# Optimization experiments

Measured on AMD Instinct MI355X. Metric: run time of the kernel, lower is better.

Reference implementation:

```python
import jax, jax.numpy as jnp
import numpy as np

B, S, D, H = 2, 2048, 1024, 16
HD = D // H


def setup_inputs() -> dict:
    key = jax.random.key(0)
    ks = jax.random.split(key, 9)
    s = 1.0 / np.sqrt(D)
    return {
        "qx": jax.random.normal(ks[0], (B, S, D), jnp.float32),
        "kx": jax.random.normal(ks[1], (B, S, D), jnp.float32),
        "vx": jax.random.normal(ks[2], (B, S, D), jnp.float32),
        "mask": jnp.tril(jnp.ones((S, S), jnp.int32))[None, None],  # [1,1,S,S] causal
        "Wq": jax.random.uniform(ks[3], (D, D), jnp.float32, -s, s),
        "bq": jax.random.uniform(ks[4], (D,), jnp.float32, -s, s),
        "Wk": jax.random.uniform(ks[5], (D, D), jnp.float32, -s, s),
        "bk": jax.random.uniform(ks[6], (D,), jnp.float32, -s, s),
        "Wv": jax.random.uniform(ks[7], (D, D), jnp.float32, -s, s),
        "bv": jax.random.uniform(ks[8], (D,), jnp.float32, -s, s),
    }


def reference(qx, kx, vx, mask, Wq, bq, Wk, bk, Wv, bv):
    bat, seq_len, d_model = qx.shape
    # torch Linear: y = x @ W.T + b
    q = qx @ Wq.T + bq
    k = kx @ Wk.T + bk
    v = vx @ Wv.T + bv
    # [b, h, s, hd]
    q = q.reshape(bat, seq_len, H, HD).transpose(0, 2, 1, 3)
    k = k.reshape(bat, seq_len, H, HD).transpose(0, 2, 1, 3)
    v = v.reshape(bat, seq_len, H, HD).transpose(0, 2, 1, 3)
    # NOTE: original scales by sqrt(d_model), not sqrt(head_dim)
    attn_weight = jnp.einsum('bhqd,bhkd->bhqk', q, k) / jnp.sqrt(
        jnp.asarray(d_model, q.dtype))
    attn_weight = jnp.where(mask == 0, -jnp.inf, attn_weight)
    attn_score = jax.nn.softmax(attn_weight, axis=-1)
    attn_output = jnp.einsum('bhqk,bhkd->bhqd', attn_score, v)
    return attn_output.transpose(0, 2, 1, 3).reshape(bat, seq_len, d_model)
```

## Files before the change

kernel.cpp:

```cpp
#include <hip/hip_runtime.h>


typedef __attribute__((ext_vector_type(8))) short short8;
typedef __attribute__((ext_vector_type(4))) short shortx4;
typedef __attribute__((ext_vector_type(4))) float floatx4;

#define NEGBIG (-1.0e30f)
#define QSCALE 0.04508422002778011f

__device__ __forceinline__ float bf2f(ushort u) {
    union { unsigned int i; float f; } x; x.i = ((unsigned int)u) << 16; return x.f;
}
__device__ __forceinline__ ushort f2bf(float f) {
    union { unsigned int i; float f; } x; x.f = f;
    return (ushort)((x.i + 0x7FFFu + ((x.i >> 16) & 1u)) >> 16);
}
__device__ __forceinline__ ushort f2bf_trunc(float f) {
    union { unsigned int i; float f; } x; x.f = f;
    return (ushort)(x.i >> 16);
}
__device__ __forceinline__ void gl_lds16(const void* g, void* l) {
    __builtin_amdgcn_global_load_lds(
        (const __attribute__((address_space(1))) unsigned int*)g,
        (__attribute__((address_space(3))) unsigned int*)l, 16, 0, 0);
}

__global__ void convert_fp32(
    const float* __restrict__ qx, const float* __restrict__ kx, const float* __restrict__ vx,
    const float* __restrict__ wq, const float* __restrict__ wk, const float* __restrict__ wv,
    const float* __restrict__ bq, const float* __restrict__ bk, const float* __restrict__ bv,
    ushort* __restrict__ dst, int* __restrict__ flag)
{
    const unsigned int* w = (const unsigned int*)qx;
    int hits = 0;
#pragma unroll
    for (int i = 0; i < 4; ++i) {
        unsigned int v = w[threadIdx.x * 4 + i];
        int e = (int)((v >> 7) & 0xFF);
        hits += (e >= 100 && e <= 135) ? 1 : 0;
    }
    __shared__ int red[4];
    for (int off = 32; off; off >>= 1) hits += __shfl_down(hits, off);
    if ((threadIdx.x & 63) == 0) red[threadIdx.x >> 6] = hits;
    __syncthreads();
    const int dt = (red[0] + red[1] + red[2] + red[3] > 512) ? 1 : 0;
    if (blockIdx.x == 0 && threadIdx.x == 0) *flag = dt;
    if (dt) return;

    const int v = blockIdx.x * 256 + threadIdx.x;
    const float* src; int off = v;
    if      (v < 1048576) { src = qx; }
    else if (v < 2097152) { src = kx; off = v - 1048576; }
    else if (v < 3145728) { src = vx; off = v - 2097152; }
    else if (v < 3407872) { src = wq; off = v - 3145728; }
    else if (v < 3670016) { src = wk; off = v - 3407872; }
    else if (v < 3932160) { src = wv; off = v - 3670016; }
    else if (v < 3932416) { src = bq; off = v - 3932160; }
    else if (v < 3932672) { src = bk; off = v - 3932416; }
    else                  { src = bv; off = v - 3932672; }
    float4 f = ((const float4*)src)[off];
    shortx4 o;
    o[0] = (short)f2bf(f.x); o[1] = (short)f2bf(f.y);
    o[2] = (short)f2bf(f.z); o[3] = (short)f2bf(f.w);
    *(shortx4*)&dst[(size_t)v * 4] = o;
}

__global__ __launch_bounds__(256, 4) void qkv_gemm(
    const void* __restrict__ Xq_, const void* __restrict__ Wq_, const void* __restrict__ bq_,
    const void* __restrict__ Xk_, const void* __restrict__ Wk_, const void* __restrict__ bk_,
    const void* __restrict__ Xv_, const void* __restrict__ Wv_, const void* __restrict__ bv_,
    const ushort* __restrict__ conv,
    ushort* __restrict__ Yq, ushort* __restrict__ Yk, ushort* __restrict__ Yv,
    const int* __restrict__ flag)
{
    const int idx = blockIdx.x;
    const int xcd = idx & 7;
    const int j   = (idx >> 3) & 7;
    const int pg  = idx >> 6;
    const int p   = pg * 8 + xcd;
    const int z   = p >> 5;
    const int m0  = (p & 31) * 128;
    const int n0  = j * 128;

    const int dt = *flag;
    const ushort* X = dt ? (const ushort*)(z == 0 ? Xq_ : z == 1 ? Xk_ : Xv_)
                         : conv + (size_t)z * 4194304;
    const ushort* W = dt ? (const ushort*)(z == 0 ? Wq_ : z == 1 ? Wk_ : Wv_)
                         : conv + 12582912 + (size_t)z * 1048576;
    const ushort* bias = dt ? (const ushort*)(z == 0 ? bq_ : z == 1 ? bk_ : bv_)
                            : conv + 15728640 + z * 1024;
    ushort* Y = (z == 0) ? Yq : (z == 1) ? Yk : Yv;
    const float oscale = (z == 0) ? QSCALE : 1.0f;

    __shared__ __align__(16) ushort As[128 * 64];
    __shared__ __align__(16) ushort Bs[128 * 64];

    const int tid  = threadIdx.x;
    const int wave = tid >> 6;
    const int lane = tid & 63;
    const int col  = lane & 15;
    const int quad = lane >> 4;
    const int wm   = (wave >> 1) * 64;
    const int wn   = (wave & 1) * 64;

    floatx4 acc[4][4] = {};

    for (int k0 = 0; k0 < 1024; k0 += 64) {
        __syncthreads();
#pragma unroll
        for (int c = 0; c < 4; ++c) {
            const int o   = c * 4096 + tid * 16;
            const int row = o >> 7;
            const int bg  = ((o >> 4) & 7) ^ (row & 7);
            gl_lds16(X + (size_t)(m0 + row) * 1024 + k0 + bg * 8, &As[o >> 1]);
            gl_lds16(W + (size_t)(n0 + row) * 1024 + k0 + bg * 8, &Bs[o >> 1]);
        }
        __syncthreads();

#pragma unroll
        for (int h = 0; h < 2; ++h) {
            short8 af[4], bf_[4];
#pragma unroll
            for (int i = 0; i < 4; ++i) {
                const int ra = wm + i * 16 + col;
                const int rb = wn + i * 16 + col;
                af[i]  = *(const short8*)&As[ra * 64 + (((h * 4 + quad) ^ (ra & 7)) * 8)];
                bf_[i] = *(const short8*)&Bs[rb * 64 + (((h * 4 + quad) ^ (rb & 7)) * 8)];
            }
#pragma unroll
            for (int i = 0; i < 4; ++i)
#pragma unroll
                for (int jj = 0; jj < 4; ++jj)
                    acc[i][jj] = __builtin_amdgcn_mfma_f32_16x16x32_bf16(af[i], bf_[jj], acc[i][jj], 0, 0, 0);
        }
    }

    if (z == 2) {
#pragma unroll
        for (int jj = 0; jj < 4; ++jj) {
            const int n = n0 + wn + jj * 16 + col;
            const float bb = bf2f(bias[n]);
#pragma unroll
            for (int i = 0; i < 4; ++i) {
                const int m = m0 + wm + i * 16 + quad * 4;
                shortx4 pk;
#pragma unroll
                for (int r = 0; r < 4; ++r) pk[r] = (short)f2bf(acc[i][jj][r] + bb);
                *(shortx4*)&Y[((size_t)(m >> 11) * 1024 + n) * 2048 + (m & 2047)] = pk;
            }
        }
    } else {
#pragma unroll
        for (int jj = 0; jj < 4; ++jj) {
            const int n = n0 + wn + jj * 16 + col;
            const float bb = bf2f(bias[n]);
#pragma unroll
            for (int i = 0; i < 4; ++i)
#pragma unroll
                for (int r = 0; r < 4; ++r) {
                    const int m = m0 + wm + i * 16 + quad * 4 + r;
                    Y[(size_t)m * 1024 + n] = f2bf((acc[i][jj][r] + bb) * oscale);
                }
        }
    }
}

#define LDP 72

__global__ __launch_bounds__(256, 4) void attn(
    const ushort* __restrict__ Q, const ushort* __restrict__ K,
    const ushort* __restrict__ Vt, void* __restrict__ O,
    const int* __restrict__ flag)
{
    const int i   = blockIdx.x;
    const int xcd = i & 7;
    const int i3  = i >> 3;
    const int run = i3 >> 5;
    const int p   = i3 & 31;
    const int qt0 = (p & 1) ? (p >> 1) : (31 - (p >> 1));
    const int qt  = (run & 1) ? (31 - qt0) : qt0;
    const int g   = xcd + 8 * run;
    const int b   = g >> 4;
    const int h   = g & 15;
    const int q0  = qt * 64;
    const int dt  = *flag;

    __shared__ __align__(16) ushort Qs[64 * 64];
    __shared__ __align__(16) ushort Ks[64 * 64];
    __shared__ __align__(16) ushort Vs[64 * 64];
    __shared__ __align__(16) ushort Ps[4][16 * LDP];

    const int tid  = threadIdx.x;
    const int wave = tid >> 6;
    const int lane = tid & 63;
    const int col  = lane & 15;
    const int quad = lane >> 4;

    const size_t qkbase = ((size_t)b * 2048) * 1024 + h * 64;
    const size_t vtbase = ((size_t)(b * 16 + h) * 64) * 2048;

    short8 ones;
#pragma unroll
    for (int ii = 0; ii < 8; ++ii) ones[ii] = (short)0x3F80;

    const int o0   = tid * 16;
    const int o1   = 4096 + tid * 16;
    const int row0 = o0 >> 7, row1 = o1 >> 7;
    const int bg0  = ((o0 >> 4) & 7) ^ (row0 & 7);
    const int bg1  = ((o1 >> 4) & 7) ^ (row1 & 7);

    gl_lds16(Q + qkbase + (size_t)(q0 + row0) * 1024 + bg0 * 8, &Qs[o0 >> 1]);
    gl_lds16(Q + qkbase + (size_t)(q0 + row1) * 1024 + bg1 * 8, &Qs[o1 >> 1]);
    gl_lds16(K + qkbase + (size_t)row0 * 1024 + bg0 * 8, &Ks[o0 >> 1]);
    gl_lds16(K + qkbase + (size_t)row1 * 1024 + bg1 * 8, &Ks[o1 >> 1]);
    gl_lds16(Vt + vtbase + (size_t)row0 * 2048 + bg0 * 8, &Vs[o0 >> 1]);
    gl_lds16(Vt + vtbase + (size_t)row1 * 2048 + bg1 * 8, &Vs[o1 >> 1]);
    __syncthreads();

    const int rq = wave * 16 + col;
    const short8 qf0 = *(const short8*)&Qs[rq * 64 + (((quad    ) ^ (col & 7)) * 8)];
    const short8 qf1 = *(const short8*)&Qs[rq * 64 + (((quad + 4) ^ (col & 7)) * 8)];

    floatx4 oacc[4] = {};
    floatx4 sacc = {};

    for (int t = 0; t <= qt; ++t) {
        floatx4 s4[4];
#pragma unroll
        for (int ct = 0; ct < 4; ++ct) {
            const int rk = ct * 16 + col;
            short8 kf0 = *(const short8*)&Ks[rk * 64 + (((quad    ) ^ (col & 7)) * 8)];
            short8 kf1 = *(const short8*)&Ks[rk * 64 + (((quad + 4) ^ (col & 7)) * 8)];
            floatx4 a = {};
            a = __builtin_amdgcn_mfma_f32_16x16x32_bf16(qf0, kf0, a, 0, 0, 0);
            a = __builtin_amdgcn_mfma_f32_16x16x32_bf16(qf1, kf1, a, 0, 0, 0);
            s4[ct] = a;
        }

        if (t == qt) {
#pragma unroll
            for (int ct = 0; ct < 4; ++ct) {
                const int kidx = ct * 16 + col;
#pragma unroll
                for (int r = 0; r < 4; ++r) {
                    const int qidx = wave * 16 + quad * 4 + r;
                    s4[ct][r] = (kidx <= qidx) ? s4[ct][r] : NEGBIG;
                }
            }
        }

#pragma unroll
        for (int ct = 0; ct < 4; ++ct)
#pragma unroll
            for (int r = 0; r < 4; ++r) {
                float pv = __builtin_exp2f(s4[ct][r]);
                Ps[wave][(quad * 4 + r) * LDP + ct * 16 + col] = f2bf_trunc(pv);
            }

        short8 pf0 = *(const short8*)&Ps[wave][col * LDP + quad * 8];
        short8 pf1 = *(const short8*)&Ps[wave][col * LDP + 32 + quad * 8];

        sacc = __builtin_amdgcn_mfma_f32_16x16x32_bf16(pf0, ones, sacc, 0, 0, 0);
        sacc = __builtin_amdgcn_mfma_f32_16x16x32_bf16(pf1, ones, sacc, 0, 0, 0);

#pragma unroll
        for (int ct = 0; ct < 4; ++ct) {
            const int rv = ct * 16 + col;
            short8 vf0 = *(const short8*)&Vs[rv * 64 + (((quad    ) ^ (rv & 7)) * 8)];
            short8 vf1 = *(const short8*)&Vs[rv * 64 + (((quad + 4) ^ (rv & 7)) * 8)];
            oacc[ct] = __builtin_amdgcn_mfma_f32_16x16x32_bf16(pf0, vf0, oacc[ct], 0, 0, 0);
            oacc[ct] = __builtin_amdgcn_mfma_f32_16x16x32_bf16(pf1, vf1, oacc[ct], 0, 0, 0);
        }

        if (t < qt) {
            const int kv1 = (t + 1) * 64;
            __syncthreads();
            gl_lds16(K + qkbase + (size_t)(kv1 + row0) * 1024 + bg0 * 8, &Ks[o0 >> 1]);
            gl_lds16(K + qkbase + (size_t)(kv1 + row1) * 1024 + bg1 * 8, &Ks[o1 >> 1]);
            gl_lds16(Vt + vtbase + (size_t)row0 * 2048 + kv1 + bg0 * 8, &Vs[o0 >> 1]);
            gl_lds16(Vt + vtbase + (size_t)row1 * 2048 + kv1 + bg1 * 8, &Vs[o1 >> 1]);
            __syncthreads();
        }
    }

#pragma unroll
    for (int r = 0; r < 4; ++r) {
        const float inv = 1.0f / sacc[r];
        const int q = q0 + wave * 16 + quad * 4 + r;
#pragma unroll
        for (int ct = 0; ct < 4; ++ct) {
            const float v = oacc[ct][r] * inv;
            const size_t oidx = ((size_t)b * 2048 + q) * 1024 + h * 64 + ct * 16 + col;
            if (dt) ((ushort*)O)[oidx] = f2bf(v);
            else    ((float*)O)[oidx]  = v;
        }
    }
}

extern "C" void kernel_launch(void* const* d_in, const int* in_sizes, int n_in,
                              void* d_out, int out_size, void* d_ws, size_t ws_size,
                              hipStream_t stream) {
    const void* qx = d_in[0];
    const void* kx = d_in[1];
    const void* vx = d_in[2];
    const void* Wq = d_in[4]; const void* bq = d_in[5];
    const void* Wk = d_in[6]; const void* bk = d_in[7];
    const void* Wv = d_in[8]; const void* bv = d_in[9];

    int*    flag = (int*)d_ws;
    ushort* conv = (ushort*)((char*)d_ws + 256);
    ushort* Qw   = (ushort*)((char*)d_ws + 256 + 31463424);
    ushort* Kw   = Qw + (size_t)4096 * 1024;
    ushort* Vtw  = Kw + (size_t)4096 * 1024;

    convert_fp32<<<15363, 256, 0, stream>>>(
        (const float*)qx, (const float*)kx, (const float*)vx,
        (const float*)Wq, (const float*)Wk, (const float*)Wv,
        (const float*)bq, (const float*)bk, (const float*)bv, conv, flag);

    qkv_gemm<<<768, 256, 0, stream>>>(qx, Wq, bq, kx, Wk, bk, vx, Wv, bv,
                                      conv, Qw, Kw, Vtw, flag);

    attn<<<1024, 256, 0, stream>>>(Qw, Kw, Vtw, d_out, flag);
}
```

Measured before the change: 199.6 us.

## Double-buffer K/V tiles in LDS and load Q fragments directly to registers

K and V LDS tiles are now double-buffered. The next tile's global→LDS loads are issued at the start of each iteration, so they overlap the QK, softmax and PV MFMA work, and one of the two per-iteration barriers is removed. Q fragments are read straight from global memory into registers instead of being staged through LDS. The padded P scratch buffer is replaced by an XOR-swizzled 64-wide layout to avoid bank conflicts without padding. LDS use per block grows to about 40 KB, which could limit occupancy.

Result: no change. 202.0 us (+1.2%).

```diff
diff --git a/kernel.cpp b/kernel.cpp
--- a/kernel.cpp
+++ b/kernel.cpp
@@ -164,8 +164,6 @@
         }
     }
 }
-
-#define LDP 72
 
 __global__ __launch_bounds__(256, 4) void attn(
     const ushort* __restrict__ Q, const ushort* __restrict__ K,
@@ -185,10 +183,9 @@
     const int q0  = qt * 64;
     const int dt  = *flag;
 
-    __shared__ __align__(16) ushort Qs[64 * 64];
-    __shared__ __align__(16) ushort Ks[64 * 64];
-    __shared__ __align__(16) ushort Vs[64 * 64];
-    __shared__ __align__(16) ushort Ps[4][16 * LDP];
+    __shared__ __align__(16) ushort Ks[2][64 * 64];
+    __shared__ __align__(16) ushort Vs[2][64 * 64];
+    __shared__ __align__(16) ushort Ps[4][16 * 64];
 
     const int tid  = threadIdx.x;
     const int wave = tid >> 6;
@@ -209,28 +206,36 @@
     const int bg0  = ((o0 >> 4) & 7) ^ (row0 & 7);
     const int bg1  = ((o1 >> 4) & 7) ^ (row1 & 7);
 
-    gl_lds16(Q + qkbase + (size_t)(q0 + row0) * 1024 + bg0 * 8, &Qs[o0 >> 1]);
-    gl_lds16(Q + qkbase + (size_t)(q0 + row1) * 1024 + bg1 * 8, &Qs[o1 >> 1]);
-    gl_lds16(K + qkbase + (size_t)row0 * 1024 + bg0 * 8, &Ks[o0 >> 1]);
-    gl_lds16(K + qkbase + (size_t)row1 * 1024 + bg1 * 8, &Ks[o1 >> 1]);
-    gl_lds16(Vt + vtbase + (size_t)row0 * 2048 + bg0 * 8, &Vs[o0 >> 1]);
-    gl_lds16(Vt + vtbase + (size_t)row1 * 2048 + bg1 * 8, &Vs[o1 >> 1]);
+    const int rq = wave * 16 + col;
+    const short8 qf0 = *(const short8*)&Q[qkbase + (size_t)(q0 + rq) * 1024 + quad * 8];
+    const short8 qf1 = *(const short8*)&Q[qkbase + (size_t)(q0 + rq) * 1024 + 32 + quad * 8];
+
+    gl_lds16(K + qkbase + (size_t)row0 * 1024 + bg0 * 8, &Ks[0][o0 >> 1]);
+    gl_lds16(K + qkbase + (size_t)row1 * 1024 + bg1 * 8, &Ks[0][o1 >> 1]);
+    gl_lds16(Vt + vtbase + (size_t)row0 * 2048 + bg0 * 8, &Vs[0][o0 >> 1]);
+    gl_lds16(Vt + vtbase + (size_t)row1 * 2048 + bg1 * 8, &Vs[0][o1 >> 1]);
     __syncthreads();
-
-    const int rq = wave * 16 + col;
-    const short8 qf0 = *(const short8*)&Qs[rq * 64 + (((quad    ) ^ (col & 7)) * 8)];
-    const short8 qf1 = *(const short8*)&Qs[rq * 64 + (((quad + 4) ^ (col & 7)) * 8)];
 
     floatx4 oacc[4] = {};
     floatx4 sacc = {};
 
     for (int t = 0; t <= qt; ++t) {
+        const int cur = t & 1;
+
+        if (t < qt) {
+            const int kv1 = (t + 1) * 64;
+            gl_lds16(K + qkbase + (size_t)(kv1 + row0) * 1024 + bg0 * 8, &Ks[cur ^ 1][o0 >> 1]);
+            gl_lds16(K + qkbase + (size_t)(kv1 + row1) * 1024 + bg1 * 8, &Ks[cur ^ 1][o1 >> 1]);
+            gl_lds16(Vt + vtbase + (size_t)row0 * 2048 + kv1 + bg0 * 8, &Vs[cur ^ 1][o0 >> 1]);
+            gl_lds16(Vt + vtbase + (size_t)row1 * 2048 + kv1 + bg1 * 8, &Vs[cur ^ 1][o1 >> 1]);
+        }
+
         floatx4 s4[4];
 #pragma unroll
         for (int ct = 0; ct < 4; ++ct) {
             const int rk = ct * 16 + col;
-            short8 kf0 = *(const short8*)&Ks[rk * 64 + (((quad    ) ^ (col & 7)) * 8)];
-            short8 kf1 = *(const short8*)&Ks[rk * 64 + (((quad + 4) ^ (col & 7)) * 8)];
+            short8 kf0 = *(const short8*)&Ks[cur][rk * 64 + (((quad    ) ^ (col & 7)) * 8)];
+            short8 kf1 = *(const short8*)&Ks[cur][rk * 64 + (((quad + 4) ^ (col & 7)) * 8)];
             floatx4 a = {};
             a = __builtin_amdgcn_mfma_f32_16x16x32_bf16(qf0, kf0, a, 0, 0, 0);
             a = __builtin_amdgcn_mfma_f32_16x16x32_bf16(qf1, kf1, a, 0, 0, 0);
@@ -254,11 +259,13 @@
 #pragma unroll
             for (int r = 0; r < 4; ++r) {
                 float pv = __builtin_exp2f(s4[ct][r]);
-                Ps[wave][(quad * 4 + r) * LDP + ct * 16 + col] = f2bf_trunc(pv);
+                const int pr  = quad * 4 + r;
+                const int blk = (ct * 2 + (col >> 3)) ^ (pr & 7);
+                Ps[wave][pr * 64 + blk * 8 + (col & 7)] = f2bf_trunc(pv);
             }
 
-        short8 pf0 = *(const short8*)&Ps[wave][col * LDP + quad * 8];
-        short8 pf1 = *(const short8*)&Ps[wave][col * LDP + 32 + quad * 8];
+        short8 pf0 = *(const short8*)&Ps[wave][col * 64 + (((quad    ) ^ (col & 7)) * 8)];
+        short8 pf1 = *(const short8*)&Ps[wave][col * 64 + (((quad + 4) ^ (col & 7)) * 8)];
 
         sacc = __builtin_amdgcn_mfma_f32_16x16x32_bf16(pf0, ones, sacc, 0, 0, 0);
         sacc = __builtin_amdgcn_mfma_f32_16x16x32_bf16(pf1, ones, sacc, 0, 0, 0);
@@ -266,21 +273,13 @@
 #pragma unroll
         for (int ct = 0; ct < 4; ++ct) {
             const int rv = ct * 16 + col;
-            short8 vf0 = *(const short8*)&Vs[rv * 64 + (((quad    ) ^ (rv & 7)) * 8)];
-            short8 vf1 = *(const short8*)&Vs[rv * 64 + (((quad + 4) ^ (rv & 7)) * 8)];
+            short8 vf0 = *(const short8*)&Vs[cur][rv * 64 + (((quad    ) ^ (rv & 7)) * 8)];
+            short8 vf1 = *(const short8*)&Vs[cur][rv * 64 + (((quad + 4) ^ (rv & 7)) * 8)];
             oacc[ct] = __builtin_amdgcn_mfma_f32_16x16x32_bf16(pf0, vf0, oacc[ct], 0, 0, 0);
             oacc[ct] = __builtin_amdgcn_mfma_f32_16x16x32_bf16(pf1, vf1, oacc[ct], 0, 0, 0);
         }
 
-        if (t < qt) {
-            const int kv1 = (t + 1) * 64;
-            __syncthreads();
-            gl_lds16(K + qkbase + (size_t)(kv1 + row0) * 1024 + bg0 * 8, &Ks[o0 >> 1]);
-            gl_lds16(K + qkbase + (size_t)(kv1 + row1) * 1024 + bg1 * 8, &Ks[o1 >> 1]);
-            gl_lds16(Vt + vtbase + (size_t)row0 * 2048 + kv1 + bg0 * 8, &Vs[o0 >> 1]);
-            gl_lds16(Vt + vtbase + (size_t)row1 * 2048 + kv1 + bg1 * 8, &Vs[o1 >> 1]);
-            __syncthreads();
-        }
+        if (t < qt) __syncthreads();
     }
 
 #pragma unroll
```
